# Kernel tuning notes

Hardware: AMD Instinct MI355X
Metric: run time of the kernel (lower is better)

Reference implementation:

```python
import jax, jax.numpy as jnp
import numpy as np

B, N, DIM = 4, 4096, 512
HEADS, DHEAD, CHUNK = 4, 128, 64
MAX_LR = 1.0
EPS = 1e-6


def rmsnorm(x):
    return x * jax.lax.rsqrt(jnp.mean(x * x, axis=-1, keepdims=True) + EPS)


def mem_mlp(params, x):
    # MemoryMLP depth=2: x @ W1 -> silu -> @ W2 (no biases)
    W1, W2 = params
    return jax.nn.silu(x @ W1) @ W2


def assoc_scan(gates, x):
    # linear recurrence y_i = g_i * y_{i-1} + x_i along axis=1 (chunks)
    def op(a, b):
        ga, xa = a
        gb, xb = b
        return (ga * gb, gb * xa + xb)
    _, y = jax.lax.associative_scan(op, (gates, x), axis=1)
    return y


def setup_inputs() -> dict:
    key = jax.random.key(0)
    ks = jax.random.split(key, 12)
    di = HEADS * DHEAD
    nrm = lambda k, shp, sc: jax.random.normal(k, shp, jnp.float32) * sc
    return {
        'seq': nrm(ks[0], (B, N, DIM), 1.0),
        'g_store': jnp.ones((DIM,), jnp.float32),
        'g_retrieve': jnp.ones((DIM,), jnp.float32),
        'W_q': nrm(ks[1], (DIM, di), DIM ** -0.5),
        'W_kv': nrm(ks[2], (DIM, 2 * di), DIM ** -0.5),
        'W_step': nrm(ks[3], (DIM, HEADS), DIM ** -0.5),
        'W_mom': nrm(ks[4], (DIM, HEADS), DIM ** -0.5),
        'W_decay': nrm(ks[5], (DIM, HEADS), DIM ** -0.5),
        'W_gate': nrm(ks[6], (DIM, HEADS), DIM ** -0.5),
        'gamma_mh': jnp.zeros((HEADS, 1, DHEAD), jnp.float32),
        'W_o': nrm(ks[7], (di, DIM), di ** -0.5),
        'M_W1': nrm(ks[8], (DHEAD, DHEAD), DHEAD ** -0.5),
        'M_W2': nrm(ks[9], (DHEAD, DHEAD), DHEAD ** -0.5),
    }


def reference(seq, g_store, g_retrieve, W_q, W_kv, W_step, W_mom, W_decay,
              W_gate, gamma_mh, W_o, M_W1, M_W2):
    b, n, dim = seq.shape
    h, d, c = HEADS, DHEAD, CHUNK
    nc = n // c
    bh = b * h

    # ---------------- store path ----------------
    s = rmsnorm(seq) * g_store                                   # (b,n,dim)
    lr = jax.nn.sigmoid(s @ W_step) * MAX_LR                     # (b,n,h)
    lr_c = lr.transpose(0, 2, 1).reshape(bh, nc, c)              # (bh,nc,c)
    chunked = s.reshape(b, nc, c, dim).mean(2)                   # (b,nc,dim)
    decay = jax.nn.sigmoid(chunked @ W_decay).transpose(0, 2, 1).reshape(bh, nc)
    mom = jax.nn.sigmoid(chunked @ W_mom).transpose(0, 2, 1).reshape(bh, nc)

    kv = s @ W_kv                                                # (b,n,2*h*d)
    k, v = jnp.split(kv, 2, axis=-1)
    to_chunks = lambda t: t.reshape(b, n, h, d).transpose(0, 2, 1, 3).reshape(bh, nc, c, d)
    k, v = to_chunks(k), to_chunks(v)

    # per-chunk gradient at the initial memory weights (vmap(grad))
    def chunk_loss(params, kc, lrc, vc):
        pred = mem_mlp(params, kc)                               # (c,d)
        loss = jnp.mean((pred - vc) ** 2, axis=-1)               # (c,)
        return jnp.sum(loss * lrc)

    gfn = jax.vmap(jax.vmap(jax.grad(chunk_loss),
                            in_axes=((None, None), 0, 0, 0)),
                   in_axes=((None, None), 0, 0, 0))
    g1, g2 = gfn((M_W1, M_W2), k, lr_c, v)                       # (bh,nc,d,d)
    s1, s2 = -g1, -g2                                            # surprises

    # momentum assoc scan: m_i = mom_i * m_{i-1} + s_i
    momg = mom[:, :, None, None]
    m1 = assoc_scan(momg, s1)
    m2 = assoc_scan(momg, s2)

    # decay-gated weight recurrence with prev = initial weights:
    # W_i = (1 - decay_i) * W_{i-1} + m_i,  W_0 = init
    def scan_with_init(gates, x, w0):
        g = jnp.concatenate([jnp.ones_like(gates[:, :1]), gates], axis=1)
        x0 = jnp.broadcast_to(w0, (bh, 1) + w0.shape)
        return assoc_scan(g, jnp.concatenate([x0, x], axis=1))   # (bh,nc+1,d,d)

    dg = (1.0 - decay)[:, :, None, None]
    u1 = scan_with_init(dg, m1, M_W1)
    u2 = scan_with_init(dg, m2, M_W2)
    # retrieval for chunk i uses weights after chunk i-1 (paper semantics)
    w1c, w2c = u1[:, :-1], u2[:, :-1]                            # (bh,nc,d,d)

    # ---------------- retrieve path ----------------
    r = rmsnorm(seq) * g_retrieve
    q = to_chunks(r @ W_q)                                       # (bh,nc,c,d)
    pred = jax.vmap(jax.vmap(lambda w1, w2, qc: mem_mlp((w1, w2), qc)))(w1c, w2c, q)
    out = pred.reshape(b, h, n, d)
    out = rmsnorm(out) * (gamma_mh + 1.0)                        # multihead rmsnorm
    gate = jax.nn.sigmoid(r @ W_gate)                            # (b,n,h)
    out = out * gate.transpose(0, 2, 1)[..., None]               # retrieve gate
    out = out.transpose(0, 2, 1, 3).reshape(b, n, h * d)         # merge heads
    return out @ W_o                                             # combine heads
```

## Files before the change

### kernel.cpp

```cpp
#include <hip/hip_runtime.h>

typedef unsigned short u16;
typedef unsigned int u32;
typedef __attribute__((ext_vector_type(8))) short s16x8;
typedef __attribute__((ext_vector_type(4))) float f32x4;

#define DEV __device__ __forceinline__
#define MFMA16(a,b,c) __builtin_amdgcn_mfma_f32_16x16x32_bf16(a,b,c,0,0,0)

DEV float bf2f(u16 x){ u32 u=((u32)x)<<16; float f; __builtin_memcpy(&f,&u,4); return f; }
DEV u16 f2bf(float f){ u32 u; __builtin_memcpy(&u,&f,4); u32 r=u+0x7FFFu+((u>>16)&1u); return (u16)(r>>16); }
DEV uint4 pack8(const float* f){
  uint4 v;
  v.x=(u32)f2bf(f[0])|((u32)f2bf(f[1])<<16);
  v.y=(u32)f2bf(f[2])|((u32)f2bf(f[3])<<16);
  v.z=(u32)f2bf(f[4])|((u32)f2bf(f[5])<<16);
  v.w=(u32)f2bf(f[6])|((u32)f2bf(f[7])<<16);
  return v;
}
DEV float sigm(float x){ return 1.0f/(1.0f+__expf(-x)); }

DEV void trans_tile(const float* src, u16* dst, int K, int Nn, int bx, int by, int tid)
{
  __shared__ float ld[64][65];
  int n0 = bx*64, k0 = by*64;
  #pragma unroll
  for (int rr=0; rr<4; rr++){
    int kk = rr*16 + (tid>>4);
    int nn = (tid&15)*4;
    float4 v = *(const float4*)(src + (size_t)(k0+kk)*Nn + n0 + nn);
    ld[kk][nn]=v.x; ld[kk][nn+1]=v.y; ld[kk][nn+2]=v.z; ld[kk][nn+3]=v.w;
  }
  __syncthreads();
  int nn2 = tid>>2, kb = (tid&3)*16;
  float o[16];
  #pragma unroll
  for (int j=0;j<16;j++) o[j] = ld[kb+j][nn2];
  u16* dp = dst + (size_t)(n0+nn2)*K + k0 + kb;
  *(uint4*)dp     = pack8(&o[0]);
  *(uint4*)(dp+8) = pack8(&o[8]);
}

__global__ __launch_bounds__(256) void k_prep(const float* __restrict__ Wkv,
    const float* __restrict__ Wq, const float* __restrict__ Wo,
    const float* __restrict__ MW1, const float* __restrict__ MW2,
    u16* __restrict__ Wkvt, u16* __restrict__ Wqt, u16* __restrict__ Wot,
    u16* __restrict__ W1t, u16* __restrict__ W2t, u16* __restrict__ W2s)
{
  int blk = blockIdx.x, tid = threadIdx.x;
  if (blk < 128)      trans_tile(Wkv, Wkvt, 512, 1024, blk&15, blk>>4, tid);
  else if (blk < 192){ int l = blk-128; trans_tile(Wq, Wqt, 512, 512, l&7, l>>3, tid); }
  else if (blk < 256){ int l = blk-192; trans_tile(Wo, Wot, 512, 512, l&7, l>>3, tid); }
  else if (blk < 260){ int l = blk-256; trans_tile(MW1, W1t, 128, 128, l&1, l>>1, tid); }
  else if (blk < 264){ int l = blk-260; trans_tile(MW2, W2t, 128, 128, l&1, l>>1, tid); }
  else {
    int e = ((blk-264)*256 + tid)*8;
    float f[8];
    *(float4*)&f[0] = *(const float4*)(MW2+e);
    *(float4*)&f[4] = *(const float4*)(MW2+e+4);
    *(uint4*)(W2s+e) = pack8(f);
  }
}

__global__ __launch_bounds__(512) void k_tokchunk(const float* __restrict__ seq,
    const float* __restrict__ gs, const float* __restrict__ gr,
    const float* __restrict__ Wstep, const float* __restrict__ Wgate,
    const float* __restrict__ Wdec, const float* __restrict__ Wmom,
    u16* __restrict__ s, u16* __restrict__ r,
    float* __restrict__ lr, float* __restrict__ gate,
    float* __restrict__ momv, float* __restrict__ dgv)
{
  __shared__ float pchunk[8][512];
  __shared__ float red[8][512];
  const int blk = blockIdx.x;
  const int b = blk >> 6, ci = blk & 63;
  const int tid = threadIdx.x;
  const int wv = tid >> 6, lane = tid & 63;
  const size_t rowbase = (size_t)b*4096 + (size_t)ci*64;

  float psum[8] = {0,0,0,0,0,0,0,0};
  #pragma unroll 1
  for (int tt=0; tt<8; tt++){
    int t = wv*8 + tt;
    const float* row = seq + (rowbase + t)*512;
    float x[8];
    *(float4*)&x[0] = *(const float4*)(row + lane*8);
    *(float4*)&x[4] = *(const float4*)(row + lane*8 + 4);
    float ss = 0.f;
    #pragma unroll
    for (int j=0;j<8;j++) ss += x[j]*x[j];
    #pragma unroll
    for (int o=32;o>=1;o>>=1) ss += __shfl_xor(ss, o, 64);
    float inv = rsqrtf(ss*(1.0f/512.0f) + 1e-6f);
    float al[4] = {0,0,0,0}, ag[4] = {0,0,0,0};
    float sv8[8], rv8[8];
    #pragma unroll
    for (int j=0;j<8;j++){
      int d = lane*8 + j;
      float sn = x[j]*inv;
      float sv = sn*gs[d];
      float rv = sn*gr[d];
      sv8[j]=sv; rv8[j]=rv;
      psum[j] += sv;
      float4 wst = *(const float4*)(Wstep + d*4);
      float4 wgt = *(const float4*)(Wgate + d*4);
      al[0]+=sv*wst.x; al[1]+=sv*wst.y; al[2]+=sv*wst.z; al[3]+=sv*wst.w;
      ag[0]+=rv*wgt.x; ag[1]+=rv*wgt.y; ag[2]+=rv*wgt.z; ag[3]+=rv*wgt.w;
    }
    *(uint4*)(s + (rowbase+t)*512 + lane*8) = pack8(sv8);
    *(uint4*)(r + (rowbase+t)*512 + lane*8) = pack8(rv8);
    #pragma unroll
    for (int o=32;o>=1;o>>=1){
      #pragma unroll
      for (int h=0;h<4;h++){ al[h] += __shfl_xor(al[h], o, 64); ag[h] += __shfl_xor(ag[h], o, 64); }
    }
    if (lane == 0){
      #pragma unroll
      for (int h=0;h<4;h++){
        lr[(rowbase+t)*4 + h]   = sigm(al[h]);
        gate[(rowbase+t)*4 + h] = sigm(ag[h]);
      }
    }
  }
  #pragma unroll
  for (int j=0;j<8;j++) pchunk[wv][lane*8+j] = psum[j];
  __syncthreads();
  {
    int d = tid;
    float mean = 0.f;
    #pragma unroll
    for (int w=0;w<8;w++) mean += pchunk[w][d];
    mean *= (1.0f/64.0f);
    #pragma unroll
    for (int h=0;h<4;h++){
      red[h][d]   = mean*Wdec[d*4+h];
      red[4+h][d] = mean*Wmom[d*4+h];
    }
  }
  __syncthreads();
  {
    float sum = 0.f;
    #pragma unroll
    for (int j=0;j<8;j++) sum += red[wv][lane*8+j];
    #pragma unroll
    for (int o=32;o>=1;o>>=1) sum += __shfl_xor(sum, o, 64);
    if (lane == 0){
      if (wv < 4) dgv[((size_t)(b*4+wv))*64 + ci]     = 1.0f - sigm(sum);
      else        momv[((size_t)(b*4+(wv-4)))*64 + ci] = sigm(sum);
    }
  }
}

template<bool OUT_BF>
__global__ __launch_bounds__(256) void k_gemm(const u16* __restrict__ A,
    const u16* __restrict__ Bt, void* __restrict__ Cv, int K, int ldc)
{
  __shared__ u16 sA[128*64];
  __shared__ u16 sB[128*64];
  const int tid = threadIdx.x;
  const int wv = tid>>6, lane = tid&63, lrow = lane&15, lk = lane>>4;
  const int wm = (wv>>1)*64, wn = (wv&1)*64;
  const int rowbase = blockIdx.y*128, colbase = blockIdx.x*128;
  const int srow = lane>>3;
  const int scol = (lane&7)*8;
  f32x4 acc[4][4] = {};
  for (int kc = 0; kc < K; kc += 64){
    __syncthreads();
    #pragma unroll
    for (int it=0; it<4; ++it){
      int seg = it*4 + wv;
      int row = seg*8 + srow;
      __builtin_amdgcn_global_load_lds(
        (const __attribute__((address_space(1))) void*)(A + (size_t)(rowbase+row)*K + kc + scol),
        (__attribute__((address_space(3))) void*)&sA[seg*512 + lane*8], 16, 0, 0);
      __builtin_amdgcn_global_load_lds(
        (const __attribute__((address_space(1))) void*)(Bt + (size_t)(colbase+row)*K + kc + scol),
        (__attribute__((address_space(3))) void*)&sB[seg*512 + lane*8], 16, 0, 0);
    }
    __syncthreads();
    #pragma unroll
    for (int k0=0;k0<2;k0++){
      s16x8 a[4], b[4];
      #pragma unroll
      for (int m=0;m<4;m++) a[m] = *(const s16x8*)&sA[(wm+m*16+lrow)*64 + k0*32 + lk*8];
      #pragma unroll
      for (int n=0;n<4;n++) b[n] = *(const s16x8*)&sB[(wn+n*16+lrow)*64 + k0*32 + lk*8];
      #pragma unroll
      for (int m=0;m<4;m++)
        #pragma unroll
        for (int n=0;n<4;n++)
          acc[m][n] = MFMA16(a[m], b[n], acc[m][n]);
    }
  }
  #pragma unroll
  for (int m=0;m<4;m++)
    #pragma unroll
    for (int n=0;n<4;n++)
      #pragma unroll
      for (int r=0;r<4;r++){
        int row = rowbase + wm + m*16 + lk*4 + r;
        int col = colbase + wn + n*16 + lrow;
        float v = acc[m][n][r];
        if (OUT_BF) ((u16*)Cv)[(size_t)row*ldc + col] = f2bf(v);
        else        ((float*)Cv)[(size_t)row*ldc + col] = v;
      }
}

__global__ __launch_bounds__(256) void k_grad(const u16* __restrict__ kv,
    const float* __restrict__ lr, const u16* __restrict__ W1t,
    const u16* __restrict__ W2t, const u16* __restrict__ W2s,
    u16* __restrict__ s1, u16* __restrict__ s2)
{
  __shared__ u16 bufR[64*132];
  __shared__ u16 bufAt[128*68];
  __shared__ u16 bufPt[128*68];
  __shared__ float lrs[64];

  const int blk = blockIdx.x;
  const int bhi = blk >> 6, ci = blk & 63;
  const int b = bhi >> 2, hd = bhi & 3;
  const int tid = threadIdx.x;
  const int wv = tid>>6, lane = tid&63, lrow = lane&15, lk = lane>>4;
  int col[2]; col[0] = wv*32 + lrow; col[1] = wv*32 + 16 + lrow;
  const size_t rowbase = (size_t)b*4096 + (size_t)ci*64;

  #pragma unroll
  for (int rep=0;rep<4;rep++){
    int lin = rep*2048 + tid*8;
    int i = lin >> 7, d = lin & 127;
    *(uint4*)&bufR[i*132 + d] = *(const uint4*)(kv + (rowbase + i)*1024 + hd*128 + d);
  }
  if (tid < 64) lrs[tid] = lr[(rowbase + tid)*4 + hd] * (2.0f/128.0f);
  u16 vreg[2][4][4];
  #pragma unroll
  for (int n=0;n<2;n++)
    #pragma unroll
    for (int m=0;m<4;m++)
      #pragma unroll
      for (int r=0;r<4;r++)
        vreg[n][m][r] = kv[(rowbase + m*16 + lk*4 + r)*1024 + 512 + hd*128 + col[n]];
  s16x8 kbf[2][2];
  #pragma unroll
  for (int n=0;n<2;n++)
    #pragma unroll
    for (int k0=0;k0<2;k0++)
      #pragma unroll
      for (int j=0;j<8;j++)
        ((u16*)&kbf[n][k0])[j] = kv[(rowbase + k0*32 + lk*8 + j)*1024 + hd*128 + col[n]];
  __syncthreads();

  float spv[4][2][4];

  {
    s16x8 wf[2][4];
    #pragma unroll
    for (int n=0;n<2;n++)
      #pragma unroll
      for (int k0=0;k0<4;k0++) wf[n][k0] = *(const s16x8*)(W1t + col[n]*128 + k0*32 + lk*8);
    f32x4 acc[4][2] = {};
    #pragma unroll
    for (int k0=0;k0<4;k0++)
      #pragma unroll
      for (int m=0;m<4;m++){
        s16x8 a = *(const s16x8*)&bufR[(m*16+lrow)*132 + k0*32 + lk*8];
        #pragma unroll
        for (int n=0;n<2;n++) acc[m][n] = MFMA16(a, wf[n][k0], acc[m][n]);
      }
    __syncthreads();
    #pragma unroll
    for (int m=0;m<4;m++)
      #pragma unroll
      for (int n=0;n<2;n++){
        int row0 = m*16 + lk*4;
        u16 av4[4];
        #pragma unroll
        for (int r=0;r<4;r++){
          float h = acc[m][n][r];
          float sg = sigm(h);
          av4[r] = f2bf(h*sg);
          spv[m][n][r] = sg*(1.0f + h*(1.0f - sg));
          bufR[(row0+r)*132 + col[n]] = av4[r];
        }
        *(uint2*)&bufAt[col[n]*68 + row0] = make_uint2(
          (u32)av4[0] | ((u32)av4[1]<<16), (u32)av4[2] | ((u32)av4[3]<<16));
      }
  }
  __syncthreads();

  {
    s16x8 wf[2][4];
    #pragma unroll
    for (int n=0;n<2;n++)
      #pragma unroll
      for (int k0=0;k0<4;k0++) wf[n][k0] = *(const s16x8*)(W2t + col[n]*128 + k0*32 + lk*8);
    f32x4 acc[4][2] = {};
    #pragma unroll
    for (int k0=0;k0<4;k0++)
      #pragma unroll
      for (int m=0;m<4;m++){
        s16x8 a = *(const s16x8*)&bufR[(m*16+lrow)*132 + k0*32 + lk*8];
        #pragma unroll
        for (int n=0;n<2;n++) acc[m][n] = MFMA16(a, wf[n][k0], acc[m][n]);
      }
    __syncthreads();
    #pragma unroll
    for (int m=0;m<4;m++)
      #pragma unroll
      for (int n=0;n<2;n++){
        int row0 = m*16 + lk*4;
        u16 dp4[4];
        #pragma unroll
        for (int r=0;r<4;r++){
          int row = row0 + r;
          float vv = bf2f(vreg[n][m][r]);
          float dp = lrs[row]*(acc[m][n][r] - vv);
          dp4[r] = f2bf(dp);
          bufR[row*132 + col[n]] = dp4[r];
        }
        *(uint2*)&bufPt[col[n]*68 + row0] = make_uint2(
          (u32)dp4[0] | ((u32)dp4[1]<<16), (u32)dp4[2] | ((u32)dp4[3]<<16));
      }
  }
  __syncthreads();

  const size_t outbase = (size_t)blk * 16384;

  f32x4 da[4][2] = {};
  {
    s16x8 wf[2][4];
    #pragma unroll
    for (int n=0;n<2;n++)
      #pragma unroll
      for (int k0=0;k0<4;k0++) wf[n][k0] = *(const s16x8*)(W2s + col[n]*128 + k0*32 + lk*8);
    #pragma unroll
    for (int k0=0;k0<4;k0++)
      #pragma unroll
      for (int m=0;m<4;m++){
        s16x8 a = *(const s16x8*)&bufR[(m*16+lrow)*132 + k0*32 + lk*8];
        #pragma unroll
        for (int n=0;n<2;n++) da[m][n] = MFMA16(a, wf[n][k0], da[m][n]);
      }
  }
  {
    f32x4 acc[8][2] = {};
    #pragma unroll
    for (int k0=0;k0<2;k0++){
      s16x8 bf0 = *(const s16x8*)&bufAt[col[0]*68 + k0*32 + lk*8];
      s16x8 bf1 = *(const s16x8*)&bufAt[col[1]*68 + k0*32 + lk*8];
      #pragma unroll
      for (int m=0;m<8;m++){
        s16x8 a = *(const s16x8*)&bufPt[(m*16+lrow)*68 + k0*32 + lk*8];
        acc[m][0] = MFMA16(a, bf0, acc[m][0]);
        acc[m][1] = MFMA16(a, bf1, acc[m][1]);
      }
    }
    #pragma unroll
    for (int m=0;m<8;m++)
      #pragma unroll
      for (int n=0;n<2;n++)
        #pragma unroll
        for (int r=0;r<4;r++)
          s2[outbase + (size_t)(m*16 + lk*4 + r)*128 + col[n]] = f2bf(-acc[m][n][r]);
  }
  __syncthreads();
  #pragma unroll
  for (int m=0;m<4;m++)
    #pragma unroll
    for (int n=0;n<2;n++){
      int row0 = m*16 + lk*4;
      u16 dh4[4];
      #pragma unroll
      for (int r=0;r<4;r++) dh4[r] = f2bf(spv[m][n][r]*da[m][n][r]);
      *(uint2*)&bufAt[col[n]*68 + row0] = make_uint2(
        (u32)dh4[0] | ((u32)dh4[1]<<16), (u32)dh4[2] | ((u32)dh4[3]<<16));
    }
  __syncthreads();

  {
    f32x4 acc[8][2] = {};
    #pragma unroll
    for (int k0=0;k0<2;k0++)
      #pragma unroll
      for (int m=0;m<8;m++){
        s16x8 a = *(const s16x8*)&bufAt[(m*16+lrow)*68 + k0*32 + lk*8];
        acc[m][0] = MFMA16(a, kbf[0][k0], acc[m][0]);
        acc[m][1] = MFMA16(a, kbf[1][k0], acc[m][1]);
      }
    #pragma unroll
    for (int m=0;m<8;m++)
      #pragma unroll
      for (int n=0;n<2;n++)
        #pragma unroll
        for (int r=0;r<4;r++)
          s1[outbase + (size_t)(m*16 + lk*4 + r)*128 + col[n]] = f2bf(-acc[m][n][r]);
  }
}

__global__ __launch_bounds__(256) void k_scan(const float* __restrict__ momv,
    const float* __restrict__ dgv, const float* __restrict__ MW1,
    const float* __restrict__ MW2, u16* __restrict__ s1w, u16* __restrict__ s2w)
{
  int bhi = blockIdx.x >> 6, eb = blockIdx.x & 63;
  int e = eb*256 + threadIdx.x;
  float u1 = MW1[(e&127)*128 + (e>>7)];
  float u2 = MW2[(e&127)*128 + (e>>7)];
  float m1 = 0.f, m2 = 0.f;
  size_t base = (size_t)bhi*64*16384 + e;
  #pragma unroll 4
  for (int t=0; t<64; t++){
    float g  = momv[bhi*64 + t];
    float dg = dgv[bhi*64 + t];
    size_t idx = base + (size_t)t*16384;
    float g1v = bf2f(s1w[idx]);
    float g2v = bf2f(s2w[idx]);
    s1w[idx] = f2bf(u1);
    s2w[idx] = f2bf(u2);
    m1 = g*m1 + g1v;
    m2 = g*m2 + g2v;
    u1 = dg*u1 + m1;
    u2 = dg*u2 + m2;
  }
}

__global__ __launch_bounds__(512) void k_retr(const u16* __restrict__ qin,
    const u16* __restrict__ w1c, const u16* __restrict__ w2c,
    const float* __restrict__ gate, const float* __restrict__ gamma,
    u16* __restrict__ outp)
{
  __shared__ u16 bufA[64*132];
  __shared__ float rsum[8][64];
  const int blk = blockIdx.x;
  const int bhi = blk >> 6, ci = blk & 63;
  const int b = bhi >> 2, hd = bhi & 3;
  const int tid = threadIdx.x;
  const int wv = tid>>6, lane = tid&63, lrow = lane&15, lk = lane>>4;
  const int nb = wv*16;
  const int colw = nb + lrow;
  const size_t rowbase = (size_t)b*4096 + (size_t)ci*64;
  const u16* w1 = w1c + (size_t)blk*16384;
  const u16* w2 = w2c + (size_t)blk*16384;

  {
    s16x8 wf[4];
    #pragma unroll
    for (int k0=0;k0<4;k0++) wf[k0] = *(const s16x8*)(w1 + colw*128 + k0*32 + lk*8);
    f32x4 acc[4] = {};
    #pragma unroll
    for (int k0=0;k0<4;k0++){
      #pragma unroll
      for (int m=0;m<4;m++){
        s16x8 a = *(const s16x8*)(qin + (rowbase + m*16+lrow)*512 + hd*128 + k0*32 + lk*8);
        acc[m] = MFMA16(a, wf[k0], acc[m]);
      }
    }
    #pragma unroll
    for (int m=0;m<4;m++){
      #pragma unroll
      for (int r=0;r<4;r++){
        float h = acc[m][r];
        bufA[(m*16+lk*4+r)*132 + colw] = f2bf(h*sigm(h));
      }
    }
  }
  __syncthreads();

  f32x4 acc[4] = {};
  {
    s16x8 wf[4];
    #pragma unroll
    for (int k0=0;k0<4;k0++) wf[k0] = *(const s16x8*)(w2 + colw*128 + k0*32 + lk*8);
    #pragma unroll
    for (int k0=0;k0<4;k0++){
      #pragma unroll
      for (int m=0;m<4;m++){
        s16x8 a = *(const s16x8*)&bufA[(m*16+lrow)*132 + k0*32 + lk*8];
        acc[m] = MFMA16(a, wf[k0], acc[m]);
      }
    }
  }
  #pragma unroll
  for (int m=0;m<4;m++){
    #pragma unroll
    for (int r=0;r<4;r++){
      float p = acc[m][r]*acc[m][r];
      p += __shfl_xor(p, 1, 64);
      p += __shfl_xor(p, 2, 64);
      p += __shfl_xor(p, 4, 64);
      p += __shfl_xor(p, 8, 64);
      if (lrow == 0) rsum[wv][m*16 + lk*4 + r] = p;
    }
  }
  __syncthreads();
  float gm = gamma[hd*128 + colw] + 1.0f;
  #pragma unroll
  for (int m=0;m<4;m++){
    #pragma unroll
    for (int r=0;r<4;r++){
      int row = m*16 + lk*4 + r;
      float sum = rsum[0][row]+rsum[1][row]+rsum[2][row]+rsum[3][row]
                + rsum[4][row]+rsum[5][row]+rsum[6][row]+rsum[7][row];
      float inv = rsqrtf(sum*(1.0f/128.0f) + 1e-6f);
      float gt = gate[(rowbase+row)*4 + hd];
      outp[(rowbase+row)*512 + hd*128 + colw] = f2bf(acc[m][r]*inv*gm*gt);
    }
  }
}

extern "C" void kernel_launch(void* const* d_in, const int* in_sizes, int n_in,
                              void* d_out, int out_size, void* d_ws, size_t ws_size,
                              hipStream_t stream)
{
  const float* seq    = (const float*)d_in[0];
  const float* gstore = (const float*)d_in[1];
  const float* gret   = (const float*)d_in[2];
  const float* W_q    = (const float*)d_in[3];
  const float* W_kv   = (const float*)d_in[4];
  const float* W_step = (const float*)d_in[5];
  const float* W_mom  = (const float*)d_in[6];
  const float* W_dec  = (const float*)d_in[7];
  const float* W_gate = (const float*)d_in[8];
  const float* gamma  = (const float*)d_in[9];
  const float* W_o    = (const float*)d_in[10];
  const float* MW1    = (const float*)d_in[11];
  const float* MW2    = (const float*)d_in[12];
  float* out = (float*)d_out;

  const size_t NS = (size_t)16384*512;
  const size_t NG = (size_t)16*64*16384;
  size_t need = (5*NS + 2*NG + 524288 + 262144 + 262144 + 3*16384)*2
              + (2*65536 + 2048)*4;
  if (ws_size < need) return;

  char* ws = (char*)d_ws;
  u16* s_bf = (u16*)ws; ws += NS*2;
  u16* r_bf = (u16*)ws; ws += NS*2;
  u16* kv_bf= (u16*)ws; ws += 2*NS*2;
  u16* q_bf = (u16*)ws; ws += NS*2;
  u16* s1   = (u16*)ws; ws += NG*2;
  u16* s2   = (u16*)ws; ws += NG*2;
  u16* Wkvt = (u16*)ws; ws += (size_t)524288*2;
  u16* Wqt  = (u16*)ws; ws += (size_t)262144*2;
  u16* Wot  = (u16*)ws; ws += (size_t)262144*2;
  u16* W1tb = (u16*)ws; ws += (size_t)16384*2;
  u16* W2tb = (u16*)ws; ws += (size_t)16384*2;
  u16* W2sb = (u16*)ws; ws += (size_t)16384*2;
  float* lr   = (float*)ws; ws += (size_t)65536*4;
  float* gatep= (float*)ws; ws += (size_t)65536*4;
  float* momv = (float*)ws; ws += 1024*4;
  float* dgv  = (float*)ws; ws += 1024*4;
  u16* outp = s_bf;

  k_prep<<<272, 256, 0, stream>>>(W_kv, W_q, W_o, MW1, MW2, Wkvt, Wqt, Wot, W1tb, W2tb, W2sb);
  k_tokchunk<<<256, 512, 0, stream>>>(seq, gstore, gret, W_step, W_gate, W_dec, W_mom,
                                      s_bf, r_bf, lr, gatep, momv, dgv);
  k_gemm<true><<<dim3(8,128), 256, 0, stream>>>(s_bf, Wkvt, kv_bf, 512, 1024);
  k_gemm<true><<<dim3(4,128), 256, 0, stream>>>(r_bf, Wqt, q_bf, 512, 512);
  k_grad<<<1024, 256, 0, stream>>>(kv_bf, lr, W1tb, W2tb, W2sb, s1, s2);
  k_scan<<<1024, 256, 0, stream>>>(momv, dgv, MW1, MW2, s1, s2);
  k_retr<<<1024, 512, 0, stream>>>(q_bf, s1, s2, gatep, gamma, outp);
  k_gemm<false><<<dim3(4,128), 256, 0, stream>>>(outp, Wot, out, 512, 512);
}
```

Baseline: 205.2 us.

## Merge KV and Q GEMMs into one launch and cut register pressure in grad kernel

The separate KV and Q projection GEMMs become one launch with 1536 blocks, and both GEMM kernels remap block indices so that consecutive blocks are spread across XCD-style groups of 8. The gradient kernel gains launch_bounds(256,4), loads weight fragments per k-step instead of holding them all in registers, defers the v and k global loads until they are used, pads the LDS row stride from 132 to 136, and reuses bufR for the dh tile so one sync is removed. The aim is to cut launch overhead, improve L2 locality, and raise occupancy in k_grad. The cost is more global loads issued closer to their use, which may expose their latency.

```diff
diff --git a/kernel.cpp b/kernel.cpp
--- a/kernel.cpp
+++ b/kernel.cpp
@@ -152,15 +152,13 @@
 }
 
 template<bool OUT_BF>
-__global__ __launch_bounds__(256) void k_gemm(const u16* __restrict__ A,
-    const u16* __restrict__ Bt, void* __restrict__ Cv, int K, int ldc)
-{
-  __shared__ u16 sA[128*64];
-  __shared__ u16 sB[128*64];
+DEV void gemm_body(const u16* A, const u16* Bt, void* Cv, int K, int ldc,
+                   int bx, int by, u16* sA, u16* sB)
+{
   const int tid = threadIdx.x;
   const int wv = tid>>6, lane = tid&63, lrow = lane&15, lk = lane>>4;
   const int wm = (wv>>1)*64, wn = (wv&1)*64;
-  const int rowbase = blockIdx.y*128, colbase = blockIdx.x*128;
+  const int rowbase = by*128, colbase = bx*128;
   const int srow = lane>>3;
   const int scol = (lane&7)*8;
   f32x4 acc[4][4] = {};
@@ -206,12 +204,40 @@
       }
 }
 
-__global__ __launch_bounds__(256) void k_grad(const u16* __restrict__ kv,
+__global__ __launch_bounds__(256) void k_gemmAB(const u16* __restrict__ A1,
+    const u16* __restrict__ B1, u16* __restrict__ C1,
+    const u16* __restrict__ A2, const u16* __restrict__ B2, u16* __restrict__ C2)
+{
+  __shared__ u16 sA[128*64];
+  __shared__ u16 sB[128*64];
+  int bid = blockIdx.x;
+  if (bid < 1024){
+    int s = (bid & 7)*128 + (bid >> 3);
+    gemm_body<true>(A1, B1, C1, 512, 1024, s & 7, s >> 3, sA, sB);
+  } else {
+    int l = bid - 1024;
+    int s = (l & 7)*64 + (l >> 3);
+    gemm_body<true>(A2, B2, C2, 512, 512, s & 3, s >> 2, sA, sB);
+  }
+}
+
+template<bool OUT_BF>
+__global__ __launch_bounds__(256) void k_gemm1(const u16* __restrict__ A,
+    const u16* __restrict__ Bt, void* __restrict__ Cv, int K, int ldc, int nbx, int cpx)
+{
+  __shared__ u16 sA[128*64];
+  __shared__ u16 sB[128*64];
+  int bid = blockIdx.x;
+  int s = (bid & 7)*cpx + (bid >> 3);
+  gemm_body<OUT_BF>(A, Bt, Cv, K, ldc, s % nbx, s / nbx, sA, sB);
+}
+
+__global__ __launch_bounds__(256,4) void k_grad(const u16* __restrict__ kv,
     const float* __restrict__ lr, const u16* __restrict__ W1t,
     const u16* __restrict__ W2t, const u16* __restrict__ W2s,
     u16* __restrict__ s1, u16* __restrict__ s2)
 {
-  __shared__ u16 bufR[64*132];
+  __shared__ u16 bufR[64*136];
   __shared__ u16 bufAt[128*68];
   __shared__ u16 bufPt[128*68];
   __shared__ float lrs[64];
@@ -223,49 +249,32 @@
   const int wv = tid>>6, lane = tid&63, lrow = lane&15, lk = lane>>4;
   int col[2]; col[0] = wv*32 + lrow; col[1] = wv*32 + 16 + lrow;
   const size_t rowbase = (size_t)b*4096 + (size_t)ci*64;
+  const u16* kvb = kv + rowbase*1024 + hd*128;
 
   #pragma unroll
   for (int rep=0;rep<4;rep++){
     int lin = rep*2048 + tid*8;
     int i = lin >> 7, d = lin & 127;
-    *(uint4*)&bufR[i*132 + d] = *(const uint4*)(kv + (rowbase + i)*1024 + hd*128 + d);
+    *(uint4*)&bufR[i*136 + d] = *(const uint4*)(kvb + (size_t)i*1024 + d);
   }
   if (tid < 64) lrs[tid] = lr[(rowbase + tid)*4 + hd] * (2.0f/128.0f);
-  u16 vreg[2][4][4];
-  #pragma unroll
-  for (int n=0;n<2;n++)
-    #pragma unroll
-    for (int m=0;m<4;m++)
-      #pragma unroll
-      for (int r=0;r<4;r++)
-        vreg[n][m][r] = kv[(rowbase + m*16 + lk*4 + r)*1024 + 512 + hd*128 + col[n]];
-  s16x8 kbf[2][2];
-  #pragma unroll
-  for (int n=0;n<2;n++)
-    #pragma unroll
-    for (int k0=0;k0<2;k0++)
-      #pragma unroll
-      for (int j=0;j<8;j++)
-        ((u16*)&kbf[n][k0])[j] = kv[(rowbase + k0*32 + lk*8 + j)*1024 + hd*128 + col[n]];
   __syncthreads();
 
   float spv[4][2][4];
 
   {
-    s16x8 wf[2][4];
-    #pragma unroll
-    for (int n=0;n<2;n++)
-      #pragma unroll
-      for (int k0=0;k0<4;k0++) wf[n][k0] = *(const s16x8*)(W1t + col[n]*128 + k0*32 + lk*8);
     f32x4 acc[4][2] = {};
     #pragma unroll
-    for (int k0=0;k0<4;k0++)
+    for (int k0=0;k0<4;k0++){
+      s16x8 w0 = *(const s16x8*)(W1t + col[0]*128 + k0*32 + lk*8);
+      s16x8 w1 = *(const s16x8*)(W1t + col[1]*128 + k0*32 + lk*8);
       #pragma unroll
       for (int m=0;m<4;m++){
-        s16x8 a = *(const s16x8*)&bufR[(m*16+lrow)*132 + k0*32 + lk*8];
-        #pragma unroll
-        for (int n=0;n<2;n++) acc[m][n] = MFMA16(a, wf[n][k0], acc[m][n]);
-      }
+        s16x8 a = *(const s16x8*)&bufR[(m*16+lrow)*136 + k0*32 + lk*8];
+        acc[m][0] = MFMA16(a, w0, acc[m][0]);
+        acc[m][1] = MFMA16(a, w1, acc[m][1]);
+      }
+    }
     __syncthreads();
     #pragma unroll
     for (int m=0;m<4;m++)
@@ -279,7 +288,7 @@
           float sg = sigm(h);
           av4[r] = f2bf(h*sg);
           spv[m][n][r] = sg*(1.0f + h*(1.0f - sg));
-          bufR[(row0+r)*132 + col[n]] = av4[r];
+          bufR[(row0+r)*136 + col[n]] = av4[r];
         }
         *(uint2*)&bufAt[col[n]*68 + row0] = make_uint2(
           (u32)av4[0] | ((u32)av4[1]<<16), (u32)av4[2] | ((u32)av4[3]<<16));
@@ -288,20 +297,26 @@
   __syncthreads();
 
   {
-    s16x8 wf[2][4];
-    #pragma unroll
-    for (int n=0;n<2;n++)
-      #pragma unroll
-      for (int k0=0;k0<4;k0++) wf[n][k0] = *(const s16x8*)(W2t + col[n]*128 + k0*32 + lk*8);
     f32x4 acc[4][2] = {};
     #pragma unroll
-    for (int k0=0;k0<4;k0++)
+    for (int k0=0;k0<4;k0++){
+      s16x8 w0 = *(const s16x8*)(W2t + col[0]*128 + k0*32 + lk*8);
+      s16x8 w1 = *(const s16x8*)(W2t + col[1]*128 + k0*32 + lk*8);
       #pragma unroll
       for (int m=0;m<4;m++){
-        s16x8 a = *(const s16x8*)&bufR[(m*16+lrow)*132 + k0*32 + lk*8];
-        #pragma unroll
-        for (int n=0;n<2;n++) acc[m][n] = MFMA16(a, wf[n][k0], acc[m][n]);
-      }
+        s16x8 a = *(const s16x8*)&bufR[(m*16+lrow)*136 + k0*32 + lk*8];
+        acc[m][0] = MFMA16(a, w0, acc[m][0]);
+        acc[m][1] = MFMA16(a, w1, acc[m][1]);
+      }
+    }
+    u16 vv[4][2][4];
+    #pragma unroll
+    for (int m=0;m<4;m++)
+      #pragma unroll
+      for (int n=0;n<2;n++)
+        #pragma unroll
+        for (int r=0;r<4;r++)
+          vv[m][n][r] = kvb[(size_t)(m*16+lk*4+r)*1024 + 512 + col[n]];
     __syncthreads();
     #pragma unroll
     for (int m=0;m<4;m++)
@@ -311,11 +326,9 @@
         u16 dp4[4];
         #pragma unroll
         for (int r=0;r<4;r++){
-          int row = row0 + r;
-          float vv = bf2f(vreg[n][m][r]);
-          float dp = lrs[row]*(acc[m][n][r] - vv);
+          float dp = lrs[row0+r]*(acc[m][n][r] - bf2f(vv[m][n][r]));
           dp4[r] = f2bf(dp);
-          bufR[row*132 + col[n]] = dp4[r];
+          bufR[(row0+r)*136 + col[n]] = dp4[r];
         }
         *(uint2*)&bufPt[col[n]*68 + row0] = make_uint2(
           (u32)dp4[0] | ((u32)dp4[1]<<16), (u32)dp4[2] | ((u32)dp4[3]<<16));
@@ -323,24 +336,43 @@
   }
   __syncthreads();
 
+  {
+    f32x4 da[4][2] = {};
+    #pragma unroll
+    for (int k0=0;k0<4;k0++){
+      s16x8 w0 = *(const s16x8*)(W2s + col[0]*128 + k0*32 + lk*8);
+      s16x8 w1 = *(const s16x8*)(W2s + col[1]*128 + k0*32 + lk*8);
+      #pragma unroll
+      for (int m=0;m<4;m++){
+        s16x8 a = *(const s16x8*)&bufR[(m*16+lrow)*136 + k0*32 + lk*8];
+        da[m][0] = MFMA16(a, w0, da[m][0]);
+        da[m][1] = MFMA16(a, w1, da[m][1]);
+      }
+    }
+    __syncthreads();
+    #pragma unroll
+    for (int m=0;m<4;m++)
+      #pragma unroll
+      for (int n=0;n<2;n++){
+        int row0 = m*16 + lk*4;
+        u16 dh4[4];
+        #pragma unroll
+        for (int r=0;r<4;r++) dh4[r] = f2bf(spv[m][n][r]*da[m][n][r]);
+        *(uint2*)&bufR[col[n]*68 + row0] = make_uint2(
+          (u32)dh4[0] | ((u32)dh4[1]<<16), (u32)dh4[2] | ((u32)dh4[3]<<16));
+      }
+  }
+
   const size_t outbase = (size_t)blk * 16384;
 
-  f32x4 da[4][2] = {};
-  {
-    s16x8 wf[2][4];
-    #pragma unroll
-    for (int n=0;n<2;n++)
-      #pragma unroll
-      for (int k0=0;k0<4;k0++) wf[n][k0] = *(const s16x8*)(W2s + col[n]*128 + k0*32 + lk*8);
-    #pragma unroll
-    for (int k0=0;k0<4;k0++)
-      #pragma unroll
-      for (int m=0;m<4;m++){
-        s16x8 a = *(const s16x8*)&bufR[(m*16+lrow)*132 + k0*32 + lk*8];
-        #pragma unroll
-        for (int n=0;n<2;n++) da[m][n] = MFMA16(a, wf[n][k0], da[m][n]);
-      }
-  }
+  s16x8 kbf[2][2];
+  #pragma unroll
+  for (int n=0;n<2;n++)
+    #pragma unroll
+    for (int k0=0;k0<2;k0++)
+      #pragma unroll
+      for (int j=0;j<8;j++)
+        ((u16*)&kbf[n][k0])[j] = kvb[(size_t)(k0*32 + lk*8 + j)*1024 + col[n]];
   {
     f32x4 acc[8][2] = {};
     #pragma unroll
@@ -363,18 +395,6 @@
           s2[outbase + (size_t)(m*16 + lk*4 + r)*128 + col[n]] = f2bf(-acc[m][n][r]);
   }
   __syncthreads();
-  #pragma unroll
-  for (int m=0;m<4;m++)
-    #pragma unroll
-    for (int n=0;n<2;n++){
-      int row0 = m*16 + lk*4;
-      u16 dh4[4];
-      #pragma unroll
-      for (int r=0;r<4;r++) dh4[r] = f2bf(spv[m][n][r]*da[m][n][r]);
-      *(uint2*)&bufAt[col[n]*68 + row0] = make_uint2(
-        (u32)dh4[0] | ((u32)dh4[1]<<16), (u32)dh4[2] | ((u32)dh4[3]<<16));
-    }
-  __syncthreads();
 
   {
     f32x4 acc[8][2] = {};
@@ -382,7 +402,7 @@
     for (int k0=0;k0<2;k0++)
       #pragma unroll
       for (int m=0;m<8;m++){
-        s16x8 a = *(const s16x8*)&bufAt[(m*16+lrow)*68 + k0*32 + lk*8];
+        s16x8 a = *(const s16x8*)&bufR[(m*16+lrow)*68 + k0*32 + lk*8];
         acc[m][0] = MFMA16(a, kbf[0][k0], acc[m][0]);
         acc[m][1] = MFMA16(a, kbf[1][k0], acc[m][1]);
       }
@@ -553,10 +573,9 @@
   k_prep<<<272, 256, 0, stream>>>(W_kv, W_q, W_o, MW1, MW2, Wkvt, Wqt, Wot, W1tb, W2tb, W2sb);
   k_tokchunk<<<256, 512, 0, stream>>>(seq, gstore, gret, W_step, W_gate, W_dec, W_mom,
                                       s_bf, r_bf, lr, gatep, momv, dgv);
-  k_gemm<true><<<dim3(8,128), 256, 0, stream>>>(s_bf, Wkvt, kv_bf, 512, 1024);
-  k_gemm<true><<<dim3(4,128), 256, 0, stream>>>(r_bf, Wqt, q_bf, 512, 512);
+  k_gemmAB<<<1536, 256, 0, stream>>>(s_bf, Wkvt, kv_bf, r_bf, Wqt, q_bf);
   k_grad<<<1024, 256, 0, stream>>>(kv_bf, lr, W1tb, W2tb, W2sb, s1, s2);
   k_scan<<<1024, 256, 0, stream>>>(momv, dgv, MW1, MW2, s1, s2);
   k_retr<<<1024, 512, 0, stream>>>(q_bf, s1, s2, gatep, gamma, outp);
-  k_gemm<false><<<dim3(4,128), 256, 0, stream>>>(outp, Wot, out, 512, 512);
-}
+  k_gemm1<false><<<512, 256, 0, stream>>>(outp, Wot, out, 512, 512, 4, 64);
+}
```

New measurement: 174.5 us. 15.0% less time.
